# Kernel optimization log

Measured on AMD Instinct MI355X. Metric: run time of the kernel, lower is better.

The kernel has to match this reference:

```python
import jax, jax.numpy as jnp
import numpy as np

# Dims: batch N, time T, joints V=9, K=5 adjacency partitions (spatial strategy, max_hop=2),
# in channels 16, out channels = coords = 3, temporal kernel 9 (ConvTranspose, stride 1, pad 4).
N, T, V, C_IN, C_OUT, K, KT = 256, 2048, 9, 16, 3, 5, 9


def setup_inputs() -> dict:
    key = jax.random.key(0)
    ks = jax.random.split(key, 6)
    pose_feats = jax.random.normal(ks[0], (N, T, V * C_IN), jnp.float32)
    # Fixed (non-trainable) multi-partition normalized adjacency A2: [K, V, V].
    # Graph values come from ted_db constants in the repo; stand-in: row-normalized random.
    A = jax.random.uniform(ks[1], (K, V, V), jnp.float32)
    A = A / jnp.sum(A, axis=-1, keepdims=True)
    # GCN 1x1 conv: in -> K*C_OUT channels
    W_gcn = jax.random.normal(ks[2], (K, C_OUT, C_IN), jnp.float32) * (1.0 / np.sqrt(C_IN))
    b_gcn = jax.random.normal(ks[3], (K, C_OUT), jnp.float32) * 0.02
    # Temporal ConvTranspose2d(C_OUT, C_OUT, kernel=(9,1), stride=(1,1), padding=(4,0));
    # torch weight layout [in, out, kH, kW]
    W_tcn = jax.random.normal(ks[4], (C_OUT, C_OUT, KT, 1), jnp.float32) * (1.0 / np.sqrt(C_OUT * KT))
    b_tcn = jax.random.normal(ks[5], (C_OUT,), jnp.float32) * 0.02
    return {"pose_feats": pose_feats, "A": A, "W_gcn": W_gcn, "b_gcn": b_gcn,
            "W_tcn": W_tcn, "b_tcn": b_tcn}


def _st_gcn_transpose(x, A, W_gcn, b_gcn, W_tcn, b_tcn):
    # x: [n, c_in, t, v]
    # 1x1 conv to K*C_OUT channels, then adjacency contraction over partitions k
    y = jnp.einsum('nctv,koc->nkotv', x, W_gcn) + b_gcn[None, :, :, None, None]
    y = jnp.einsum('nkotv,kvw->notw', y, A)  # [n, c_out, t, v]
    # temporal transposed conv, kernel (9,1), stride 1, torch padding 4 -> jax pad (4,4)
    y = jax.lax.conv_transpose(y, W_tcn, strides=(1, 1), padding=[(4, 4), (0, 0)],
                               dimension_numbers=('NCHW', 'IOHW', 'NCHW'),
                               transpose_kernel=True)
    y = y + b_tcn[None, :, None, None]
    return jax.nn.leaky_relu(y, 0.01)


def reference(pose_feats, A, W_gcn, b_gcn, W_tcn, b_tcn):
    n, t, f = pose_feats.shape
    x = pose_feats.reshape(n, t, V, C_IN).transpose(0, 3, 1, 2)  # [n, c_in, t, v]
    y = _st_gcn_transpose(x, A, W_gcn, b_gcn, W_tcn, b_tcn)      # [n, c_out, t, v]
    return y.transpose(0, 2, 3, 1).reshape(n, t, V * C_OUT)       # [n, t, 27]
```

## Files before the change

kernel.cpp:

```cpp
#include <hip/hip_runtime.h>

typedef short short8 __attribute__((ext_vector_type(8)));
typedef float f32x4  __attribute__((ext_vector_type(4)));

constexpr int N_    = 256;
constexpr int T_    = 2048;
constexpr int V_    = 9;
constexpr int FIN_  = 144;
constexpr int J_    = 27;
constexpr int KT_   = 9;
constexpr int THREADS_ = 256;
constexpr int TILE_ = 248;
constexpr int NTILE_ = 9;
constexpr int ZROWS_ = 256;
constexpr int XROWS_ = 64;
constexpr int XSTRIDE_B = 384;
constexpr int XBUF_B = XROWS_ * XSTRIDE_B;
constexpr int ZS_ = 28;
constexpr int ZBUF_B = ZROWS_ * ZS_ * 4;

constexpr int BF_OFF_F = 0;
constexpr int B0_OFF   = 2560;
constexpr int WT_OFF   = 2587;
constexpr int BT_OFF   = 2668;

__device__ __forceinline__ unsigned short bf16_rne(float x) {
    unsigned u = __float_as_uint(x);
    u = (u + 0x7FFFu + ((u >> 16) & 1u)) >> 16;
    return (unsigned short)u;
}
__device__ __forceinline__ unsigned pk2(float a, float b) {
    return (unsigned)bf16_rne(a) | ((unsigned)bf16_rne(b) << 16);
}

__global__ void setup_weights(const float* __restrict__ A,
                              const float* __restrict__ Wg,
                              const float* __restrict__ bg,
                              const float* __restrict__ Wt_in,
                              const float* __restrict__ bt,
                              float* __restrict__ ws) {
    __shared__ float Wc[FIN_ * J_];
    const int tid = threadIdx.x;
    for (int idx = tid; idx < FIN_ * J_; idx += 256) {
        const int f = idx / J_, j = idx % J_;
        const int v = f >> 4, c = f & 15;
        const int w = j / 3, o = j % 3;
        float s = 0.f;
        #pragma unroll
        for (int k = 0; k < 5; ++k)
            s += Wg[(k * 3 + o) * 16 + c] * A[(k * 9 + v) * 9 + w];
        Wc[idx] = s;
    }
    __syncthreads();
    unsigned short* bfp = (unsigned short*)(ws + BF_OFF_F);
    for (int i = tid; i < 5120; i += 256) {
        const int e = i & 7, lane = (i >> 3) & 63, nt = (i >> 9) & 1, s = i >> 10;
        const int k = s * 32 + (lane >> 4) * 8 + e;
        const int n = nt * 16 + (lane & 15);
        const float val = (k < FIN_ && n < J_) ? Wc[k * J_ + n] : 0.f;
        bfp[i] = bf16_rne(val);
    }
    if (tid < J_) {
        const int w = tid / 3, o = tid % 3;
        float s = 0.f;
        #pragma unroll
        for (int k = 0; k < 5; ++k) {
            float cs = 0.f;
            #pragma unroll
            for (int v = 0; v < V_; ++v) cs += A[(k * 9 + v) * 9 + w];
            s += bg[k * 3 + o] * cs;
        }
        ws[B0_OFF + tid] = s;
    }
    if (tid < 81) {
        const int o = tid / 27, r = tid % 27, o2 = r / 9, dd = r % 9;
        ws[WT_OFF + tid] = Wt_in[(o2 * 3 + o) * 9 + (8 - dd)];
    }
    if (tid < 3) ws[BT_OFF + tid] = bt[tid];
}

__global__ __launch_bounds__(THREADS_) void fused_stgcn(const float* __restrict__ pose,
                                                        const float* __restrict__ cw,
                                                        float* __restrict__ out) {
    __shared__ __align__(16) unsigned char smem[XBUF_B + ZBUF_B];
    float* zbuf = (float*)(smem + XBUF_B);

    const int tid  = threadIdx.x;
    const int bid  = blockIdx.x;
    const int nb   = bid / NTILE_;
    const int tile = bid % NTILE_;
    const int t0   = tile * TILE_;
    const int lane = tid & 63;
    const int wv   = tid >> 6;

    {
        f32x4 z4 = {0.f, 0.f, 0.f, 0.f};
        f32x4* p = (f32x4*)smem;
        for (int i = tid; i < XBUF_B / 16; i += THREADS_) p[i] = z4;
    }
    short8 bfrag[5][2];
    {
        const short8* bsrc = (const short8*)(cw + BF_OFF_F);
        #pragma unroll
        for (int s = 0; s < 5; ++s)
            #pragma unroll
            for (int nt = 0; nt < 2; ++nt)
                bfrag[s][nt] = bsrc[(s * 2 + nt) * 64 + lane];
    }
    float b0n0 = cw[B0_OFF + (lane & 15)];
    float b0n1 = (16 + (lane & 15) < J_) ? cw[B0_OFF + 16 + (lane & 15)] : 0.f;
    __syncthreads();

    for (int h = 0; h < 4; ++h) {
        float4 ld[9];
        #pragma unroll
        for (int q = 0; q < 9; ++q) {
            const int g = q * THREADS_ + tid;
            const int r = g / 36;
            const int c4 = g % 36;
            const int text = t0 - 4 + h * 64 + r;
            const bool ok = (text >= 0 && text < T_);
            ld[q] = ok ? *(const float4*)(pose + ((size_t)nb * T_ + text) * FIN_ + c4 * 4)
                       : make_float4(0.f, 0.f, 0.f, 0.f);
        }
        #pragma unroll
        for (int q = 0; q < 9; ++q) {
            const int g = q * THREADS_ + tid;
            const int r = g / 36;
            const int c4 = g % 36;
            const int blk = (c4 >> 1) ^ (r & 7);
            uint2 u;
            u.x = pk2(ld[q].x, ld[q].y);
            u.y = pk2(ld[q].z, ld[q].w);
            *(uint2*)(smem + r * XSTRIDE_B + blk * 16 + (c4 & 1) * 8) = u;
        }
        __syncthreads();

        f32x4 acc0 = {0.f, 0.f, 0.f, 0.f};
        f32x4 acc1 = {0.f, 0.f, 0.f, 0.f};
        const int arow = wv * 16 + (lane & 15);
        const int g8   = lane >> 4;
        #pragma unroll
        for (int s = 0; s < 5; ++s) {
            const int blk = (s * 4 + g8) ^ (arow & 7);
            short8 afrag = *(const short8*)(smem + arow * XSTRIDE_B + blk * 16);
            acc0 = __builtin_amdgcn_mfma_f32_16x16x32_bf16(afrag, bfrag[s][0], acc0, 0, 0, 0);
            acc1 = __builtin_amdgcn_mfma_f32_16x16x32_bf16(afrag, bfrag[s][1], acc1, 0, 0, 0);
        }
        #pragma unroll
        for (int r = 0; r < 4; ++r) {
            const int zrow = h * 64 + wv * 16 + g8 * 4 + r;
            const int text = t0 - 4 + zrow;
            const bool ok = (text >= 0 && text < T_);
            const int j0 = lane & 15;
            zbuf[zrow * ZS_ + j0] = ok ? acc0[r] + b0n0 : 0.f;
            if (16 + j0 < J_)
                zbuf[zrow * ZS_ + 16 + j0] = ok ? acc1[r] + b0n1 : 0.f;
        }
        __syncthreads();
    }

    const int rows_out = min(TILE_, T_ - t0);
    float oacc[J_];
    if (tid < rows_out) {
        #pragma unroll
        for (int w = 0; w < V_; ++w)
            #pragma unroll
            for (int o2 = 0; o2 < 3; ++o2)
                oacc[w * 3 + o2] = cw[BT_OFF + o2];
        #pragma unroll
        for (int dd = 0; dd < KT_; ++dd) {
            union { f32x4 v4[7]; float f[28]; } zu;
            const f32x4* zp = (const f32x4*)&zbuf[(tid + dd) * ZS_];
            #pragma unroll
            for (int c = 0; c < 7; ++c) zu.v4[c] = zp[c];
            #pragma unroll
            for (int o = 0; o < 3; ++o) {
                #pragma unroll
                for (int o2 = 0; o2 < 3; ++o2) {
                    const float wt = cw[WT_OFF + o * 27 + o2 * 9 + dd];
                    #pragma unroll
                    for (int w = 0; w < V_; ++w)
                        oacc[w * 3 + o2] = fmaf(zu.f[w * 3 + o], wt, oacc[w * 3 + o2]);
                }
            }
        }
        #pragma unroll
        for (int j = 0; j < J_; ++j) oacc[j] = fmaxf(oacc[j], 0.01f * oacc[j]);
    }
    __syncthreads();
    if (tid < rows_out) {
        #pragma unroll
        for (int j = 0; j < J_; ++j) zbuf[tid * J_ + j] = oacc[j];
    }
    __syncthreads();

    const int total4 = (rows_out * J_) / 4;
    float4* dst4 = (float4*)(out + ((size_t)nb * T_ + t0) * J_);
    const float4* src4 = (const float4*)zbuf;
    for (int idx = tid; idx < total4; idx += THREADS_)
        dst4[idx] = src4[idx];
}

extern "C" void kernel_launch(void* const* d_in, const int* in_sizes, int n_in,
                              void* d_out, int out_size, void* d_ws, size_t ws_size,
                              hipStream_t stream) {
    const float* pose = (const float*)d_in[0];
    const float* A    = (const float*)d_in[1];
    const float* Wg   = (const float*)d_in[2];
    const float* bg   = (const float*)d_in[3];
    const float* Wt   = (const float*)d_in[4];
    const float* bt   = (const float*)d_in[5];
    float* ws   = (float*)d_ws;
    float* outp = (float*)d_out;

    setup_weights<<<1, 256, 0, stream>>>(A, Wg, bg, Wt, bt, ws);
    fused_stgcn<<<N_ * NTILE_, THREADS_, 0, stream>>>(pose, ws, outp);
}
```

Baseline: 90.25 us.

## Load MFMA A-fragments directly from global into registers, drop LDS staging

Each wave now loads its own pose rows straight from global memory in the MFMA A-fragment layout and converts them to bf16 in registers. This removes the swizzled LDS X buffer, its zero-fill, and the per-chunk barriers. The next tile's loads are issued before the current MFMAs run, a software-prefetch scheme. Global accesses are less coalesced (two float4 per row segment per lane) and use more registers, but the freed LDS can raise occupancy.

```diff
diff --git a/kernel.cpp b/kernel.cpp
--- a/kernel.cpp
+++ b/kernel.cpp
@@ -13,9 +13,6 @@
 constexpr int TILE_ = 248;
 constexpr int NTILE_ = 9;
 constexpr int ZROWS_ = 256;
-constexpr int XROWS_ = 64;
-constexpr int XSTRIDE_B = 384;
-constexpr int XBUF_B = XROWS_ * XSTRIDE_B;
 constexpr int ZS_ = 28;
 constexpr int ZBUF_B = ZROWS_ * ZS_ * 4;
 
@@ -82,8 +79,7 @@
 __global__ __launch_bounds__(THREADS_) void fused_stgcn(const float* __restrict__ pose,
                                                         const float* __restrict__ cw,
                                                         float* __restrict__ out) {
-    __shared__ __align__(16) unsigned char smem[XBUF_B + ZBUF_B];
-    float* zbuf = (float*)(smem + XBUF_B);
+    __shared__ __align__(16) float zbuf[ZROWS_ * ZS_];
 
     const int tid  = threadIdx.x;
     const int bid  = blockIdx.x;
@@ -92,12 +88,9 @@
     const int t0   = tile * TILE_;
     const int lane = tid & 63;
     const int wv   = tid >> 6;
-
-    {
-        f32x4 z4 = {0.f, 0.f, 0.f, 0.f};
-        f32x4* p = (f32x4*)smem;
-        for (int i = tid; i < XBUF_B / 16; i += THREADS_) p[i] = z4;
-    }
+    const int g8   = lane >> 4;
+    const int j0   = lane & 15;
+
     short8 bfrag[5][2];
     {
         const short8* bsrc = (const short8*)(cw + BF_OFF_F);
@@ -107,58 +100,58 @@
             for (int nt = 0; nt < 2; ++nt)
                 bfrag[s][nt] = bsrc[(s * 2 + nt) * 64 + lane];
     }
-    float b0n0 = cw[B0_OFF + (lane & 15)];
-    float b0n1 = (16 + (lane & 15) < J_) ? cw[B0_OFF + 16 + (lane & 15)] : 0.f;
-    __syncthreads();
-
-    for (int h = 0; h < 4; ++h) {
-        float4 ld[9];
-        #pragma unroll
-        for (int q = 0; q < 9; ++q) {
-            const int g = q * THREADS_ + tid;
-            const int r = g / 36;
-            const int c4 = g % 36;
-            const int text = t0 - 4 + h * 64 + r;
-            const bool ok = (text >= 0 && text < T_);
-            ld[q] = ok ? *(const float4*)(pose + ((size_t)nb * T_ + text) * FIN_ + c4 * 4)
-                       : make_float4(0.f, 0.f, 0.f, 0.f);
-        }
-        #pragma unroll
-        for (int q = 0; q < 9; ++q) {
-            const int g = q * THREADS_ + tid;
-            const int r = g / 36;
-            const int c4 = g % 36;
-            const int blk = (c4 >> 1) ^ (r & 7);
-            uint2 u;
-            u.x = pk2(ld[q].x, ld[q].y);
-            u.y = pk2(ld[q].z, ld[q].w);
-            *(uint2*)(smem + r * XSTRIDE_B + blk * 16 + (c4 & 1) * 8) = u;
-        }
-        __syncthreads();
+    const float b0n0 = cw[B0_OFF + j0];
+    const float b0n1 = (j0 < 11) ? cw[B0_OFF + 16 + j0] : 0.f;
+
+    const size_t nrow0 = (size_t)nb * T_;
+
+    float4 pA[5], pB[5];
+    auto issue = [&](int mt, float4* Av, float4* Bv) {
+        const int text = t0 - 4 + wv * 64 + mt * 16 + j0;
+        const bool okr = (text >= 0 && text < T_);
+        const float* rowp = pose + (nrow0 + (okr ? text : 0)) * FIN_;
+        #pragma unroll
+        for (int s = 0; s < 5; ++s) {
+            const int k0 = s * 32 + g8 * 8;
+            const bool ok = okr && (k0 < FIN_);
+            Av[s] = ok ? *(const float4*)(rowp + k0)     : make_float4(0.f, 0.f, 0.f, 0.f);
+            Bv[s] = ok ? *(const float4*)(rowp + k0 + 4) : make_float4(0.f, 0.f, 0.f, 0.f);
+        }
+    };
+
+    issue(0, pA, pB);
+    #pragma unroll
+    for (int mt = 0; mt < 4; ++mt) {
+        short8 af[5];
+        #pragma unroll
+        for (int s = 0; s < 5; ++s) {
+            union { unsigned u[4]; short8 s8; } cvu;
+            cvu.u[0] = pk2(pA[s].x, pA[s].y);
+            cvu.u[1] = pk2(pA[s].z, pA[s].w);
+            cvu.u[2] = pk2(pB[s].x, pB[s].y);
+            cvu.u[3] = pk2(pB[s].z, pB[s].w);
+            af[s] = cvu.s8;
+        }
+        if (mt < 3) issue(mt + 1, pA, pB);
 
         f32x4 acc0 = {0.f, 0.f, 0.f, 0.f};
         f32x4 acc1 = {0.f, 0.f, 0.f, 0.f};
-        const int arow = wv * 16 + (lane & 15);
-        const int g8   = lane >> 4;
         #pragma unroll
         for (int s = 0; s < 5; ++s) {
-            const int blk = (s * 4 + g8) ^ (arow & 7);
-            short8 afrag = *(const short8*)(smem + arow * XSTRIDE_B + blk * 16);
-            acc0 = __builtin_amdgcn_mfma_f32_16x16x32_bf16(afrag, bfrag[s][0], acc0, 0, 0, 0);
-            acc1 = __builtin_amdgcn_mfma_f32_16x16x32_bf16(afrag, bfrag[s][1], acc1, 0, 0, 0);
+            acc0 = __builtin_amdgcn_mfma_f32_16x16x32_bf16(af[s], bfrag[s][0], acc0, 0, 0, 0);
+            acc1 = __builtin_amdgcn_mfma_f32_16x16x32_bf16(af[s], bfrag[s][1], acc1, 0, 0, 0);
         }
         #pragma unroll
         for (int r = 0; r < 4; ++r) {
-            const int zrow = h * 64 + wv * 16 + g8 * 4 + r;
+            const int zrow = wv * 64 + mt * 16 + g8 * 4 + r;
             const int text = t0 - 4 + zrow;
-            const bool ok = (text >= 0 && text < T_);
-            const int j0 = lane & 15;
-            zbuf[zrow * ZS_ + j0] = ok ? acc0[r] + b0n0 : 0.f;
-            if (16 + j0 < J_)
-                zbuf[zrow * ZS_ + 16 + j0] = ok ? acc1[r] + b0n1 : 0.f;
-        }
-        __syncthreads();
-    }
+            const bool okz = (text >= 0 && text < T_);
+            zbuf[zrow * ZS_ + j0] = okz ? acc0[r] + b0n0 : 0.f;
+            if (j0 < 11)
+                zbuf[zrow * ZS_ + 16 + j0] = okz ? acc1[r] + b0n1 : 0.f;
+        }
+    }
+    __syncthreads();
 
     const int rows_out = min(TILE_, T_ - t0);
     float oacc[J_];
@@ -196,7 +189,7 @@
     __syncthreads();
 
     const int total4 = (rows_out * J_) / 4;
-    float4* dst4 = (float4*)(out + ((size_t)nb * T_ + t0) * J_);
+    float4* dst4 = (float4*)(out + (nrow0 + t0) * J_);
     const float4* src4 = (const float4*)zbuf;
     for (int idx = tid; idx < total4; idx += THREADS_)
         dst4[idx] = src4[idx];
```

Measured after the change: 87.24 us. 1.03x faster.
